# Optimization experiments

Measured on AMD Instinct MI355X. Metric: run time of the kernel, lower is better.

The kernel has to match this reference:

```python
import jax, jax.numpy as jnp
import numpy as np

D_EMB = 1024
N_H = 16
D_H = D_EMB // N_H

def setup_inputs() -> dict:
    key = jax.random.key(0)
    ks = jax.random.split(key, 9)
    s = 1.0 / np.sqrt(D_EMB)
    inp = {"x": jax.random.normal(ks[0], (2, 2048, D_EMB), dtype=jnp.float32)}
    for i, name in enumerate(["q", "k", "v", "o"]):
        inp[f"W{name}"] = jax.random.uniform(ks[1 + 2 * i], (D_EMB, D_EMB), minval=-s, maxval=s, dtype=jnp.float32)
        inp[f"b{name}"] = jax.random.uniform(ks[2 + 2 * i], (D_EMB,), minval=-s, maxval=s, dtype=jnp.float32)
    return inp

def reference(x, Wq, bq, Wk, bk, Wv, bv, Wo, bo):
    B, S, D = x.shape
    # torch Linear: y = x @ W.T + b
    Q = x @ Wq.T + bq
    K = x @ Wk.T + bk
    V = x @ Wv.T + bv
    # [B, H, S, d_h]
    Qh = Q.reshape(B, S, N_H, D_H).transpose(0, 2, 1, 3)
    Kh = K.reshape(B, S, N_H, D_H).transpose(0, 2, 1, 3)
    Vh = V.reshape(B, S, N_H, D_H).transpose(0, 2, 1, 3)
    scores = jnp.einsum("bhsd,bhtd->bhst", Qh, Kh) / jnp.sqrt(jnp.float32(D_H))
    causal = jnp.tril(jnp.ones((S, S), dtype=bool))
    scores = jnp.where(causal, scores, -jnp.inf)
    attn = jax.nn.softmax(scores, axis=-1)
    out = jnp.einsum("bhst,bhtd->bhsd", attn, Vh)
    out = out.transpose(0, 2, 1, 3).reshape(B, S, D)
    return out @ Wo.T + bo
```

## Files before the change

kernel.cpp:

```cpp
#include <hip/hip_runtime.h>
#include <stdint.h>

#define B_  2
#define S_  2048
#define D_  1024
#define H_  16
#define DH_ 64
#define M_  (B_ * S_)

#define NEG_BIG   (-1.0e30f)
#define EXP_FLOOR (-60.0f)
#define FIXED_M   16.0f

typedef uint16_t u16;
typedef uint32_t u32;
typedef u16   u16x4  __attribute__((ext_vector_type(4)));
typedef u16   u16x8  __attribute__((ext_vector_type(8)));
typedef u32   u32x4  __attribute__((ext_vector_type(4)));
typedef __bf16 bf16_t;
typedef bf16_t bf16x8 __attribute__((ext_vector_type(8)));
typedef float floatx4 __attribute__((ext_vector_type(4)));

__device__ __forceinline__ u16 f2b(float f) {
  u32 u = __float_as_uint(f);
  return (u16)((u + 0x7FFFu + ((u >> 16) & 1u)) >> 16);
}
__device__ __forceinline__ bf16x8 bc8(u16x8 v) { return __builtin_bit_cast(bf16x8, v); }

__device__ __forceinline__ void async16(u16* lds, const u16* g) {
  __builtin_amdgcn_global_load_lds(
      (const __attribute__((address_space(1))) u32*)g,
      (__attribute__((address_space(3))) u32*)lds, 16, 0, 0);
}

__global__ __launch_bounds__(256) void cvt_kernel(
    const float* __restrict__ X,
    const float* __restrict__ Wq, const float* __restrict__ Wk,
    const float* __restrict__ Wv, const float* __restrict__ Wo,
    u16* __restrict__ Xb, u16* __restrict__ Wqb, u16* __restrict__ Wkb,
    u16* __restrict__ Wvb, u16* __restrict__ Wob)
{
  const int XC = (M_ * D_) / 8;
  const int WC = (D_ * D_) / 8;
  const int total = XC + 4 * WC;
  for (int cid = blockIdx.x * 256 + threadIdx.x; cid < total; cid += gridDim.x * 256) {
    const float* src; u16* dst; int off;
    if (cid < XC)               { src = X;  dst = Xb;  off = cid; }
    else if (cid < XC + WC)     { src = Wq; dst = Wqb; off = cid - XC; }
    else if (cid < XC + 2 * WC) { src = Wk; dst = Wkb; off = cid - XC - WC; }
    else if (cid < XC + 3 * WC) { src = Wv; dst = Wvb; off = cid - XC - 2 * WC; }
    else                        { src = Wo; dst = Wob; off = cid - XC - 3 * WC; }
    const float4* p = (const float4*)(src + (size_t)off * 8);
    float4 lo = p[0], hi = p[1];
    u16x8 o;
    o[0] = f2b(lo.x); o[1] = f2b(lo.y); o[2] = f2b(lo.z); o[3] = f2b(lo.w);
    o[4] = f2b(hi.x); o[5] = f2b(hi.y); o[6] = f2b(hi.z); o[7] = f2b(hi.w);
    *(u16x8*)(dst + (size_t)off * 8) = o;
  }
}

__global__ __launch_bounds__(256) void qkv_kernel(
    const u16* __restrict__ Xb,
    const u16* __restrict__ Wqb, const u16* __restrict__ Wkb, const u16* __restrict__ Wvb,
    const float* __restrict__ bq, const float* __restrict__ bk, const float* __restrict__ bv,
    u16* __restrict__ Qb, u16* __restrict__ Kb, u16* __restrict__ Vb)
{
  const int which = blockIdx.y >> 3;
  const u16* W      = (which == 0) ? Wqb : (which == 1) ? Wkb : Wvb;
  const float* bias = (which == 0) ? bq : (which == 1) ? bk : bv;
  u16* Y            = (which == 0) ? Qb : (which == 1) ? Kb : Vb;
  const int gm = blockIdx.x * 128;
  const int gn = (blockIdx.y & 7) * 128;

  __shared__ u16 Al[2][128][32];
  __shared__ u16 Bl[2][128][32];

  const int t  = threadIdx.x;
  const int wv = t >> 6, ln = t & 63;
  const int c  = ln & 15, g = ln >> 4;
  const int wm = (wv >> 1) * 64, wn = (wv & 1) * 64;

  const int srow   = ln >> 2;
  const int schunk = (ln & 3) ^ ((ln >> 3) & 3);
  const u16* a0 = Xb + (size_t)(gm + wv * 16 + srow) * D_ + schunk * 8;
  const u16* a1 = a0 + (size_t)64 * D_;
  const u16* b0 = W  + (size_t)(gn + wv * 16 + srow) * D_ + schunk * 8;
  const u16* b1 = b0 + (size_t)64 * D_;

  floatx4 acc[4][4] = {};
  const int rsw = (c >> 1) & 3;

  async16(&Al[0][wv * 16][0],      a0);
  async16(&Al[0][64 + wv * 16][0], a1);
  async16(&Bl[0][wv * 16][0],      b0);
  async16(&Bl[0][64 + wv * 16][0], b1);

  for (int kt = 0; kt < D_ / 32; ++kt) {
    __syncthreads();
    if (kt + 1 < D_ / 32) {
      const int nb = (kt + 1) & 1;
      const int ko = (kt + 1) * 32;
      async16(&Al[nb][wv * 16][0],      a0 + ko);
      async16(&Al[nb][64 + wv * 16][0], a1 + ko);
      async16(&Bl[nb][wv * 16][0],      b0 + ko);
      async16(&Bl[nb][64 + wv * 16][0], b1 + ko);
    }
    const int bf = kt & 1;
    bf16x8 am[4], bn[4];
#pragma unroll
    for (int i = 0; i < 4; ++i) {
      am[i] = bc8(*(const u16x8*)&Al[bf][wm + 16 * i + c][(g ^ rsw) * 8]);
      bn[i] = bc8(*(const u16x8*)&Bl[bf][wn + 16 * i + c][(g ^ rsw) * 8]);
    }
#pragma unroll
    for (int mi = 0; mi < 4; ++mi)
#pragma unroll
      for (int ni = 0; ni < 4; ++ni)
        acc[mi][ni] = __builtin_amdgcn_mfma_f32_16x16x32_bf16(am[mi], bn[ni], acc[mi][ni], 0, 0, 0);
  }

#pragma unroll
  for (int ni = 0; ni < 4; ++ni) {
    const int col = gn + wn + 16 * ni + c;
    const float bv_ = bias[col];
#pragma unroll
    for (int mi = 0; mi < 4; ++mi)
#pragma unroll
      for (int r = 0; r < 4; ++r)
        Y[(size_t)(gm + wm + 16 * mi + 4 * g + r) * D_ + col] = f2b(acc[mi][ni][r] + bv_);
  }
}

__global__ __launch_bounds__(256) void proj_kernel(
    const u16* __restrict__ A, const u16* __restrict__ Wb,
    const float* __restrict__ bias, float* __restrict__ Y)
{
  const int gm = blockIdx.x * 64;
  const int gn = blockIdx.y * 128;

  __shared__ u16 Al[2][64][32];
  __shared__ u16 Bl[2][128][32];

  const int t  = threadIdx.x;
  const int wv = t >> 6, ln = t & 63;
  const int c  = ln & 15, g = ln >> 4;
  const int wm = (wv >> 1) * 32, wn = (wv & 1) * 64;

  const int srow   = ln >> 2;
  const int schunk = (ln & 3) ^ ((ln >> 3) & 3);
  const u16* a0 = A  + (size_t)(gm + wv * 16 + srow) * D_ + schunk * 8;
  const u16* b0 = Wb + (size_t)(gn + wv * 16 + srow) * D_ + schunk * 8;
  const u16* b1 = b0 + (size_t)64 * D_;

  floatx4 acc[2][4] = {};
  const int rsw = (c >> 1) & 3;

  async16(&Al[0][wv * 16][0],      a0);
  async16(&Bl[0][wv * 16][0],      b0);
  async16(&Bl[0][64 + wv * 16][0], b1);

  for (int kt = 0; kt < D_ / 32; ++kt) {
    __syncthreads();
    if (kt + 1 < D_ / 32) {
      const int nb = (kt + 1) & 1;
      const int ko = (kt + 1) * 32;
      async16(&Al[nb][wv * 16][0],      a0 + ko);
      async16(&Bl[nb][wv * 16][0],      b0 + ko);
      async16(&Bl[nb][64 + wv * 16][0], b1 + ko);
    }
    const int bf = kt & 1;
    bf16x8 am[2], bn[4];
#pragma unroll
    for (int i = 0; i < 2; ++i)
      am[i] = bc8(*(const u16x8*)&Al[bf][wm + 16 * i + c][(g ^ rsw) * 8]);
#pragma unroll
    for (int i = 0; i < 4; ++i)
      bn[i] = bc8(*(const u16x8*)&Bl[bf][wn + 16 * i + c][(g ^ rsw) * 8]);
#pragma unroll
    for (int mi = 0; mi < 2; ++mi)
#pragma unroll
      for (int ni = 0; ni < 4; ++ni)
        acc[mi][ni] = __builtin_amdgcn_mfma_f32_16x16x32_bf16(am[mi], bn[ni], acc[mi][ni], 0, 0, 0);
  }

#pragma unroll
  for (int ni = 0; ni < 4; ++ni) {
    const int col = gn + wn + 16 * ni + c;
    const float bv_ = bias[col];
#pragma unroll
    for (int mi = 0; mi < 2; ++mi)
#pragma unroll
      for (int r = 0; r < 4; ++r)
        Y[(size_t)(gm + wm + 16 * mi + 4 * g + r) * D_ + col] = acc[mi][ni][r] + bv_;
  }
}

__global__ __launch_bounds__(256) void attn_kernel(
    const u16* __restrict__ Qg, const u16* __restrict__ Kg,
    const u16* __restrict__ Vg, u16* __restrict__ Og)
{
  const int bh = blockIdx.x;
  const int b = bh >> 4, h = bh & 15;
  const int qb = 31 - blockIdx.y;
  const int q0 = qb * 64;

  __shared__ u16 Kl[64][72];
  __shared__ u16 Vt[64][72];

  const int t = threadIdx.x;
  const int wave = t >> 6, lane = t & 63;
  const int c = lane & 15, g = lane >> 4;
  const int qrow = q0 + wave * 16 + c;

  bf16x8 qf[2];
  {
    const u16* qsrc = Qg + (size_t)(b * S_ + qrow) * D_ + h * DH_ + 8 * g;
    qf[0] = bc8(*(const u16x8*)qsrc);
    qf[1] = bc8(*(const u16x8*)(qsrc + 32));
  }

  float l_run = 0.f;
  floatx4 o[4] = {};

  const int kr = t >> 2, kc = (t & 3) * 16;
  const int vkp = t & 31, vdg = t >> 5;

  u16x8 kreg0, kreg1;
  u32 vpack[8];
  {
    const u16* ksrc = Kg + (size_t)(b * S_ + kr) * D_ + h * DH_ + kc;
    kreg0 = *(const u16x8*)ksrc;
    kreg1 = *(const u16x8*)(ksrc + 8);
    const u16* vsrc = Vg + (size_t)(b * S_ + 2 * vkp) * D_ + h * DH_ + 8 * vdg;
    u16x8 va = *(const u16x8*)vsrc;
    u16x8 vb2 = *(const u16x8*)(vsrc + D_);
#pragma unroll
    for (int i = 0; i < 8; ++i) vpack[i] = (u32)va[i] | ((u32)vb2[i] << 16);
  }

  for (int kt = 0; kt <= qb; ++kt) {
    const int k0 = kt * 64;
    __syncthreads();
    *(u16x8*)&Kl[kr][kc]     = kreg0;
    *(u16x8*)&Kl[kr][kc + 8] = kreg1;
#pragma unroll
    for (int i = 0; i < 8; ++i) *(u32*)&Vt[8 * vdg + i][2 * vkp] = vpack[i];
    __syncthreads();

    if (kt < qb) {
      const u16* ksrc = Kg + (size_t)(b * S_ + k0 + 64 + kr) * D_ + h * DH_ + kc;
      kreg0 = *(const u16x8*)ksrc;
      kreg1 = *(const u16x8*)(ksrc + 8);
      const u16* vsrc = Vg + (size_t)(b * S_ + k0 + 64 + 2 * vkp) * D_ + h * DH_ + 8 * vdg;
      u16x8 va = *(const u16x8*)vsrc;
      u16x8 vb2 = *(const u16x8*)(vsrc + D_);
#pragma unroll
      for (int i = 0; i < 8; ++i) vpack[i] = (u32)va[i] | ((u32)vb2[i] << 16);
    }

    floatx4 st[4] = {};
#pragma unroll
    for (int mb = 0; mb < 4; ++mb) {
      bf16x8 a0 = bc8(*(const u16x8*)&Kl[16 * mb + c][8 * g]);
      bf16x8 a1 = bc8(*(const u16x8*)&Kl[16 * mb + c][32 + 8 * g]);
      st[mb] = __builtin_amdgcn_mfma_f32_16x16x32_bf16(a0, qf[0], st[mb], 0, 0, 0);
      st[mb] = __builtin_amdgcn_mfma_f32_16x16x32_bf16(a1, qf[1], st[mb], 0, 0, 0);
    }

    u32 plo[4], phi[4];
    float psum = 0.f;
    const bool diag = (kt == qb);
#pragma unroll
    for (int mb = 0; mb < 4; ++mb) {
      u32 pb[4];
#pragma unroll
      for (int r = 0; r < 4; ++r) {
        float arg = fmaf(st[mb][r], 0.125f, -FIXED_M);
        if (diag && (k0 + 16 * mb + 4 * g + r > qrow)) arg = NEG_BIG;
        arg = fmaxf(arg, EXP_FLOOR);
        float p = __expf(arg);
        pb[r] = __float_as_uint(p) & 0xFFFF0000u;
        psum += __uint_as_float(pb[r]);
      }
      plo[mb] = (pb[0] >> 16) | pb[1];
      phi[mb] = (pb[2] >> 16) | pb[3];
    }
    l_run += psum;

    const int s1 = c + 32 * (g & 1);
    const int s2 = s1 + 16;
    const bool hi = (g >= 2);
#pragma unroll
    for (int ks = 0; ks < 2; ++ks) {
      u32 q0a = (u32)__shfl((int)plo[2 * ks],     s1);
      u32 q1a = (u32)__shfl((int)phi[2 * ks],     s1);
      u32 q2a = (u32)__shfl((int)plo[2 * ks],     s2);
      u32 q3a = (u32)__shfl((int)phi[2 * ks],     s2);
      u32 q0b = (u32)__shfl((int)plo[2 * ks + 1], s1);
      u32 q1b = (u32)__shfl((int)phi[2 * ks + 1], s1);
      u32 q2b = (u32)__shfl((int)plo[2 * ks + 1], s2);
      u32 q3b = (u32)__shfl((int)phi[2 * ks + 1], s2);
      u32x4 pa = { hi ? q0b : q0a, hi ? q1b : q1a, hi ? q2b : q2a, hi ? q3b : q3a };
      bf16x8 pfrag = __builtin_bit_cast(bf16x8, pa);
#pragma unroll
      for (int nb = 0; nb < 4; ++nb) {
        bf16x8 vf = bc8(*(const u16x8*)&Vt[16 * nb + c][32 * ks + 8 * g]);
        o[nb] = __builtin_amdgcn_mfma_f32_16x16x32_bf16(vf, pfrag, o[nb], 0, 0, 0);
      }
    }
  }

  l_run += __shfl_xor(l_run, 16);
  l_run += __shfl_xor(l_run, 32);
  const float inv = 1.0f / l_run;
#pragma unroll
  for (int nb = 0; nb < 4; ++nb) {
    u16x4 ov;
#pragma unroll
    for (int r = 0; r < 4; ++r) ov[r] = f2b(o[nb][r] * inv);
    *(u16x4*)(Og + (size_t)(b * S_ + qrow) * D_ + h * DH_ + 16 * nb + 4 * g) = ov;
  }
}

extern "C" void kernel_launch(void* const* d_in, const int* in_sizes, int n_in,
                              void* d_out, int out_size, void* d_ws, size_t ws_size,
                              hipStream_t stream) {
  const float* x  = (const float*)d_in[0];
  const float* Wq = (const float*)d_in[1];
  const float* bq = (const float*)d_in[2];
  const float* Wk = (const float*)d_in[3];
  const float* bk = (const float*)d_in[4];
  const float* Wv = (const float*)d_in[5];
  const float* bv = (const float*)d_in[6];
  const float* Wo = (const float*)d_in[7];
  const float* bo = (const float*)d_in[8];

  u16* Xb  = (u16*)d_ws;
  u16* Wqb = Xb  + (size_t)M_ * D_;
  u16* Wkb = Wqb + (size_t)D_ * D_;
  u16* Wvb = Wkb + (size_t)D_ * D_;
  u16* Wob = Wvb + (size_t)D_ * D_;
  u16* Qb  = Wob + (size_t)D_ * D_;
  u16* Vb  = (u16*)d_out;
  u16* Kb  = Vb + (size_t)M_ * D_;

  cvt_kernel<<<dim3(2048), 256, 0, stream>>>(x, Wq, Wk, Wv, Wo, Xb, Wqb, Wkb, Wvb, Wob);
  qkv_kernel<<<dim3(32, 24), 256, 0, stream>>>(Xb, Wqb, Wkb, Wvb, bq, bk, bv, Qb, Kb, Vb);
  attn_kernel<<<dim3(B_ * H_, 32), 256, 0, stream>>>(Qb, Kb, Vb, Qb);
  proj_kernel<<<dim3(64, 8), 256, 0, stream>>>(Qb, Wob, bo, (float*)d_out);
}
```

Before: 194.0 us.

## Process two query sub-tiles per wave in attention with fewer threads

The attention kernel now runs 2 waves per block instead of 4, and each wave handles 32 query rows (two 16-row subtiles). K and V fragments loaded from LDS are reused across both subtiles, and each thread stages twice as much K/V data. The softmax uses exp2 with a pre-scaled constant, drops the exponent floor clamp, converts to bf16 with a packed hardware convert, and is specialised for diagonal versus off-diagonal tiles. The permutation shuffle is reworked to need 4 shuffles per subtile instead of 8. Register pressure rises and there are fewer waves per block to hide latency.

```diff
diff --git a/kernel.cpp b/kernel.cpp
--- a/kernel.cpp
+++ b/kernel.cpp
@@ -9,7 +9,6 @@
 #define M_  (B_ * S_)
 
 #define NEG_BIG   (-1.0e30f)
-#define EXP_FLOOR (-60.0f)
 #define FIXED_M   16.0f
 
 typedef uint16_t u16;
@@ -195,7 +194,7 @@
   }
 }
 
-__global__ __launch_bounds__(256) void attn_kernel(
+__global__ __launch_bounds__(128) void attn_kernel(
     const u16* __restrict__ Qg, const u16* __restrict__ Kg,
     const u16* __restrict__ Vg, u16* __restrict__ Og)
 {
@@ -208,117 +207,149 @@
   __shared__ u16 Vt[64][72];
 
   const int t = threadIdx.x;
-  const int wave = t >> 6, lane = t & 63;
+  const int w = t >> 6, lane = t & 63;
   const int c = lane & 15, g = lane >> 4;
-  const int qrow = q0 + wave * 16 + c;
-
-  bf16x8 qf[2];
-  {
-    const u16* qsrc = Qg + (size_t)(b * S_ + qrow) * D_ + h * DH_ + 8 * g;
-    qf[0] = bc8(*(const u16x8*)qsrc);
-    qf[1] = bc8(*(const u16x8*)(qsrc + 32));
-  }
-
-  float l_run = 0.f;
-  floatx4 o[4] = {};
-
-  const int kr = t >> 2, kc = (t & 3) * 16;
+  const int qbase = q0 + 32 * w;
+
+  const float C1 = 0.125f * 1.44269504f;
+  const float C2 = -FIXED_M * 1.44269504f;
+
+  bf16x8 qf[2][2];
+#pragma unroll
+  for (int qs = 0; qs < 2; ++qs) {
+    const u16* qsrc = Qg + (size_t)(b * S_ + qbase + 16 * qs + c) * D_ + h * DH_ + 8 * g;
+    qf[qs][0] = bc8(*(const u16x8*)qsrc);
+    qf[qs][1] = bc8(*(const u16x8*)(qsrc + 32));
+  }
+
+  float l_run[2] = {0.f, 0.f};
+  floatx4 o[2][4] = {};
+
+  const int kr = t >> 1, kc = (t & 1) * 32;
   const int vkp = t & 31, vdg = t >> 5;
 
-  u16x8 kreg0, kreg1;
-  u32 vpack[8];
+  u16x8 kreg[4];
+  u32 vpack[16];
   {
     const u16* ksrc = Kg + (size_t)(b * S_ + kr) * D_ + h * DH_ + kc;
-    kreg0 = *(const u16x8*)ksrc;
-    kreg1 = *(const u16x8*)(ksrc + 8);
-    const u16* vsrc = Vg + (size_t)(b * S_ + 2 * vkp) * D_ + h * DH_ + 8 * vdg;
-    u16x8 va = *(const u16x8*)vsrc;
-    u16x8 vb2 = *(const u16x8*)(vsrc + D_);
-#pragma unroll
-    for (int i = 0; i < 8; ++i) vpack[i] = (u32)va[i] | ((u32)vb2[i] << 16);
-  }
+#pragma unroll
+    for (int i = 0; i < 4; ++i) kreg[i] = *(const u16x8*)(ksrc + 8 * i);
+    const u16* vsrc = Vg + (size_t)(b * S_ + 2 * vkp) * D_ + h * DH_ + 16 * vdg;
+    u16x8 va0 = *(const u16x8*)vsrc;
+    u16x8 va1 = *(const u16x8*)(vsrc + 8);
+    u16x8 vb0 = *(const u16x8*)(vsrc + D_);
+    u16x8 vb1 = *(const u16x8*)(vsrc + D_ + 8);
+#pragma unroll
+    for (int i = 0; i < 8; ++i) {
+      vpack[i]     = (u32)va0[i] | ((u32)vb0[i] << 16);
+      vpack[8 + i] = (u32)va1[i] | ((u32)vb1[i] << 16);
+    }
+  }
+
+  u32 plo[2][4], phi[2][4];
 
   for (int kt = 0; kt <= qb; ++kt) {
     const int k0 = kt * 64;
     __syncthreads();
-    *(u16x8*)&Kl[kr][kc]     = kreg0;
-    *(u16x8*)&Kl[kr][kc + 8] = kreg1;
-#pragma unroll
-    for (int i = 0; i < 8; ++i) *(u32*)&Vt[8 * vdg + i][2 * vkp] = vpack[i];
+#pragma unroll
+    for (int i = 0; i < 4; ++i) *(u16x8*)&Kl[kr][kc + 8 * i] = kreg[i];
+#pragma unroll
+    for (int i = 0; i < 16; ++i) *(u32*)&Vt[16 * vdg + i][2 * vkp] = vpack[i];
     __syncthreads();
 
     if (kt < qb) {
       const u16* ksrc = Kg + (size_t)(b * S_ + k0 + 64 + kr) * D_ + h * DH_ + kc;
-      kreg0 = *(const u16x8*)ksrc;
-      kreg1 = *(const u16x8*)(ksrc + 8);
-      const u16* vsrc = Vg + (size_t)(b * S_ + k0 + 64 + 2 * vkp) * D_ + h * DH_ + 8 * vdg;
-      u16x8 va = *(const u16x8*)vsrc;
-      u16x8 vb2 = *(const u16x8*)(vsrc + D_);
-#pragma unroll
-      for (int i = 0; i < 8; ++i) vpack[i] = (u32)va[i] | ((u32)vb2[i] << 16);
-    }
-
-    floatx4 st[4] = {};
+#pragma unroll
+      for (int i = 0; i < 4; ++i) kreg[i] = *(const u16x8*)(ksrc + 8 * i);
+      const u16* vsrc = Vg + (size_t)(b * S_ + k0 + 64 + 2 * vkp) * D_ + h * DH_ + 16 * vdg;
+      u16x8 va0 = *(const u16x8*)vsrc;
+      u16x8 va1 = *(const u16x8*)(vsrc + 8);
+      u16x8 vb0 = *(const u16x8*)(vsrc + D_);
+      u16x8 vb1 = *(const u16x8*)(vsrc + D_ + 8);
+#pragma unroll
+      for (int i = 0; i < 8; ++i) {
+        vpack[i]     = (u32)va0[i] | ((u32)vb0[i] << 16);
+        vpack[8 + i] = (u32)va1[i] | ((u32)vb1[i] << 16);
+      }
+    }
+
+    floatx4 st[2][4] = {};
 #pragma unroll
     for (int mb = 0; mb < 4; ++mb) {
       bf16x8 a0 = bc8(*(const u16x8*)&Kl[16 * mb + c][8 * g]);
       bf16x8 a1 = bc8(*(const u16x8*)&Kl[16 * mb + c][32 + 8 * g]);
-      st[mb] = __builtin_amdgcn_mfma_f32_16x16x32_bf16(a0, qf[0], st[mb], 0, 0, 0);
-      st[mb] = __builtin_amdgcn_mfma_f32_16x16x32_bf16(a1, qf[1], st[mb], 0, 0, 0);
-    }
-
-    u32 plo[4], phi[4];
-    float psum = 0.f;
-    const bool diag = (kt == qb);
-#pragma unroll
-    for (int mb = 0; mb < 4; ++mb) {
-      u32 pb[4];
-#pragma unroll
-      for (int r = 0; r < 4; ++r) {
-        float arg = fmaf(st[mb][r], 0.125f, -FIXED_M);
-        if (diag && (k0 + 16 * mb + 4 * g + r > qrow)) arg = NEG_BIG;
-        arg = fmaxf(arg, EXP_FLOOR);
-        float p = __expf(arg);
-        pb[r] = __float_as_uint(p) & 0xFFFF0000u;
-        psum += __uint_as_float(pb[r]);
+      st[0][mb] = __builtin_amdgcn_mfma_f32_16x16x32_bf16(a0, qf[0][0], st[0][mb], 0, 0, 0);
+      st[0][mb] = __builtin_amdgcn_mfma_f32_16x16x32_bf16(a1, qf[0][1], st[0][mb], 0, 0, 0);
+      st[1][mb] = __builtin_amdgcn_mfma_f32_16x16x32_bf16(a0, qf[1][0], st[1][mb], 0, 0, 0);
+      st[1][mb] = __builtin_amdgcn_mfma_f32_16x16x32_bf16(a1, qf[1][1], st[1][mb], 0, 0, 0);
+    }
+
+    auto softmax = [&](bool DIAG) {
+#pragma unroll
+      for (int qs = 0; qs < 2; ++qs) {
+        const int qrow_ = qbase + 16 * qs + c;
+        float psum = 0.f;
+#pragma unroll
+        for (int mb = 0; mb < 4; ++mb) {
+          float p[4];
+#pragma unroll
+          for (int r = 0; r < 4; ++r) {
+            float arg = fmaf(st[qs][mb][r], C1, C2);
+            if (DIAG && (k0 + 16 * mb + 4 * g + r > qrow_)) arg = NEG_BIG;
+            p[r] = __builtin_exp2f(arg);
+            psum += p[r];
+          }
+          asm("v_cvt_pk_bf16_f32 %0, %1, %2" : "=v"(plo[qs][mb]) : "v"(p[0]), "v"(p[1]));
+          asm("v_cvt_pk_bf16_f32 %0, %1, %2" : "=v"(phi[qs][mb]) : "v"(p[2]), "v"(p[3]));
+        }
+        l_run[qs] += psum;
       }
-      plo[mb] = (pb[0] >> 16) | pb[1];
-      phi[mb] = (pb[2] >> 16) | pb[3];
-    }
-    l_run += psum;
-
-    const int s1 = c + 32 * (g & 1);
-    const int s2 = s1 + 16;
-    const bool hi = (g >= 2);
+    };
+    if (kt == qb) softmax(true); else softmax(false);
+
+    const int gb = g & 1, gh = g >> 1;
+    const int aA = c + 32 * gb + 16 * gh;
+    const int aB = c + 32 * gb + 16 * (1 - gh);
 #pragma unroll
     for (int ks = 0; ks < 2; ++ks) {
-      u32 q0a = (u32)__shfl((int)plo[2 * ks],     s1);
-      u32 q1a = (u32)__shfl((int)phi[2 * ks],     s1);
-      u32 q2a = (u32)__shfl((int)plo[2 * ks],     s2);
-      u32 q3a = (u32)__shfl((int)phi[2 * ks],     s2);
-      u32 q0b = (u32)__shfl((int)plo[2 * ks + 1], s1);
-      u32 q1b = (u32)__shfl((int)phi[2 * ks + 1], s1);
-      u32 q2b = (u32)__shfl((int)plo[2 * ks + 1], s2);
-      u32 q3b = (u32)__shfl((int)phi[2 * ks + 1], s2);
-      u32x4 pa = { hi ? q0b : q0a, hi ? q1b : q1a, hi ? q2b : q2a, hi ? q3b : q3a };
-      bf16x8 pfrag = __builtin_bit_cast(bf16x8, pa);
+      bf16x8 pfrag[2];
+#pragma unroll
+      for (int qs = 0; qs < 2; ++qs) {
+        u32 x0 = gb ? plo[qs][2 * ks + 1] : plo[qs][2 * ks];
+        u32 x1 = gb ? phi[qs][2 * ks + 1] : phi[qs][2 * ks];
+        u32 x2 = gb ? plo[qs][2 * ks]     : plo[qs][2 * ks + 1];
+        u32 x3 = gb ? phi[qs][2 * ks]     : phi[qs][2 * ks + 1];
+        u32 i0 = (u32)__shfl((int)x0, aA);
+        u32 i1 = (u32)__shfl((int)x1, aA);
+        u32 i2 = (u32)__shfl((int)x2, aB);
+        u32 i3 = (u32)__shfl((int)x3, aB);
+        const bool sw = (gh != 0);
+        u32x4 pa = { sw ? i2 : i0, sw ? i3 : i1, sw ? i0 : i2, sw ? i1 : i3 };
+        pfrag[qs] = __builtin_bit_cast(bf16x8, pa);
+      }
 #pragma unroll
       for (int nb = 0; nb < 4; ++nb) {
         bf16x8 vf = bc8(*(const u16x8*)&Vt[16 * nb + c][32 * ks + 8 * g]);
-        o[nb] = __builtin_amdgcn_mfma_f32_16x16x32_bf16(vf, pfrag, o[nb], 0, 0, 0);
+        o[0][nb] = __builtin_amdgcn_mfma_f32_16x16x32_bf16(vf, pfrag[0], o[0][nb], 0, 0, 0);
+        o[1][nb] = __builtin_amdgcn_mfma_f32_16x16x32_bf16(vf, pfrag[1], o[1][nb], 0, 0, 0);
       }
     }
   }
 
-  l_run += __shfl_xor(l_run, 16);
-  l_run += __shfl_xor(l_run, 32);
-  const float inv = 1.0f / l_run;
-#pragma unroll
-  for (int nb = 0; nb < 4; ++nb) {
-    u16x4 ov;
-#pragma unroll
-    for (int r = 0; r < 4; ++r) ov[r] = f2b(o[nb][r] * inv);
-    *(u16x4*)(Og + (size_t)(b * S_ + qrow) * D_ + h * DH_ + 16 * nb + 4 * g) = ov;
+#pragma unroll
+  for (int qs = 0; qs < 2; ++qs) {
+    float l = l_run[qs];
+    l += __shfl_xor(l, 16);
+    l += __shfl_xor(l, 32);
+    const float inv = 1.0f / l;
+    const int qrow_ = qbase + 16 * qs + c;
+#pragma unroll
+    for (int nb = 0; nb < 4; ++nb) {
+      u16x4 ov;
+#pragma unroll
+      for (int r = 0; r < 4; ++r) ov[r] = f2b(o[qs][nb][r] * inv);
+      *(u16x4*)(Og + (size_t)(b * S_ + qrow_) * D_ + h * DH_ + 16 * nb + 4 * g) = ov;
+    }
   }
 }
 
@@ -346,6 +377,6 @@
 
   cvt_kernel<<<dim3(2048), 256, 0, stream>>>(x, Wq, Wk, Wv, Wo, Xb, Wqb, Wkb, Wvb, Wob);
   qkv_kernel<<<dim3(32, 24), 256, 0, stream>>>(Xb, Wqb, Wkb, Wvb, bq, bk, bv, Qb, Kb, Vb);
-  attn_kernel<<<dim3(B_ * H_, 32), 256, 0, stream>>>(Qb, Kb, Vb, Qb);
+  attn_kernel<<<dim3(B_ * H_, 32), 128, 0, stream>>>(Qb, Kb, Vb, Qb);
   proj_kernel<<<dim3(64, 8), 256, 0, stream>>>(Qb, Wob, bo, (float*)d_out);
 }
```

Measured after the change: 207.2 us. 6.8% more time.

## Double-buffer K/V LDS tiles and streamline softmax exp and P shuffles

Applied to the files above, without the earlier changes.

Double-buffers the K and V LDS tiles so each iteration needs one barrier instead of two, letting stores for the next tile proceed without waiting on readers of the previous one. The softmax is rewritten to use exp2 with pre-folded log2e constants, drops the exp floor clamp, and converts pairs with the hardware packed bf16 conversion instead of truncation masks. A mask-free softmax variant is used for non-diagonal tiles. The P redistribution halves the number of cross-lane shuffles by pre-selecting sources. Rounding now differs slightly from truncation, and removing the clamp relies on exp2 underflowing cleanly to zero.

```diff
diff --git a/kernel.cpp b/kernel.cpp
--- a/kernel.cpp
+++ b/kernel.cpp
@@ -9,7 +9,6 @@
 #define M_  (B_ * S_)
 
 #define NEG_BIG   (-1.0e30f)
-#define EXP_FLOOR (-60.0f)
 #define FIXED_M   16.0f
 
 typedef uint16_t u16;
@@ -204,13 +203,16 @@
   const int qb = 31 - blockIdx.y;
   const int q0 = qb * 64;
 
-  __shared__ u16 Kl[64][72];
-  __shared__ u16 Vt[64][72];
+  __shared__ u16 Kl[2][64][72];
+  __shared__ u16 Vt[2][64][72];
 
   const int t = threadIdx.x;
   const int wave = t >> 6, lane = t & 63;
   const int c = lane & 15, g = lane >> 4;
   const int qrow = q0 + wave * 16 + c;
+
+  const float C1 = 0.125f * 1.44269504f;
+  const float C2 = -FIXED_M * 1.44269504f;
 
   bf16x8 qf[2];
   {
@@ -225,86 +227,85 @@
   const int kr = t >> 2, kc = (t & 3) * 16;
   const int vkp = t & 31, vdg = t >> 5;
 
-  u16x8 kreg0, kreg1;
-  u32 vpack[8];
+  u16x8 kreg0, kreg1, va, vb2;
   {
     const u16* ksrc = Kg + (size_t)(b * S_ + kr) * D_ + h * DH_ + kc;
     kreg0 = *(const u16x8*)ksrc;
     kreg1 = *(const u16x8*)(ksrc + 8);
     const u16* vsrc = Vg + (size_t)(b * S_ + 2 * vkp) * D_ + h * DH_ + 8 * vdg;
-    u16x8 va = *(const u16x8*)vsrc;
-    u16x8 vb2 = *(const u16x8*)(vsrc + D_);
-#pragma unroll
-    for (int i = 0; i < 8; ++i) vpack[i] = (u32)va[i] | ((u32)vb2[i] << 16);
+    va  = *(const u16x8*)vsrc;
+    vb2 = *(const u16x8*)(vsrc + D_);
   }
 
   for (int kt = 0; kt <= qb; ++kt) {
     const int k0 = kt * 64;
-    __syncthreads();
-    *(u16x8*)&Kl[kr][kc]     = kreg0;
-    *(u16x8*)&Kl[kr][kc + 8] = kreg1;
-#pragma unroll
-    for (int i = 0; i < 8; ++i) *(u32*)&Vt[8 * vdg + i][2 * vkp] = vpack[i];
-    __syncthreads();
+    const int bf = kt & 1;
+
+    *(u16x8*)&Kl[bf][kr][kc]     = kreg0;
+    *(u16x8*)&Kl[bf][kr][kc + 8] = kreg1;
+#pragma unroll
+    for (int i = 0; i < 8; ++i)
+      *(u32*)&Vt[bf][8 * vdg + i][2 * vkp] = (u32)va[i] | ((u32)vb2[i] << 16);
 
     if (kt < qb) {
       const u16* ksrc = Kg + (size_t)(b * S_ + k0 + 64 + kr) * D_ + h * DH_ + kc;
       kreg0 = *(const u16x8*)ksrc;
       kreg1 = *(const u16x8*)(ksrc + 8);
       const u16* vsrc = Vg + (size_t)(b * S_ + k0 + 64 + 2 * vkp) * D_ + h * DH_ + 8 * vdg;
-      u16x8 va = *(const u16x8*)vsrc;
-      u16x8 vb2 = *(const u16x8*)(vsrc + D_);
-#pragma unroll
-      for (int i = 0; i < 8; ++i) vpack[i] = (u32)va[i] | ((u32)vb2[i] << 16);
-    }
+      va  = *(const u16x8*)vsrc;
+      vb2 = *(const u16x8*)(vsrc + D_);
+    }
+
+    __syncthreads();
 
     floatx4 st[4] = {};
 #pragma unroll
     for (int mb = 0; mb < 4; ++mb) {
-      bf16x8 a0 = bc8(*(const u16x8*)&Kl[16 * mb + c][8 * g]);
-      bf16x8 a1 = bc8(*(const u16x8*)&Kl[16 * mb + c][32 + 8 * g]);
+      bf16x8 a0 = bc8(*(const u16x8*)&Kl[bf][16 * mb + c][8 * g]);
+      bf16x8 a1 = bc8(*(const u16x8*)&Kl[bf][16 * mb + c][32 + 8 * g]);
       st[mb] = __builtin_amdgcn_mfma_f32_16x16x32_bf16(a0, qf[0], st[mb], 0, 0, 0);
       st[mb] = __builtin_amdgcn_mfma_f32_16x16x32_bf16(a1, qf[1], st[mb], 0, 0, 0);
     }
 
     u32 plo[4], phi[4];
-    float psum = 0.f;
-    const bool diag = (kt == qb);
-#pragma unroll
-    for (int mb = 0; mb < 4; ++mb) {
-      u32 pb[4];
-#pragma unroll
-      for (int r = 0; r < 4; ++r) {
-        float arg = fmaf(st[mb][r], 0.125f, -FIXED_M);
-        if (diag && (k0 + 16 * mb + 4 * g + r > qrow)) arg = NEG_BIG;
-        arg = fmaxf(arg, EXP_FLOOR);
-        float p = __expf(arg);
-        pb[r] = __float_as_uint(p) & 0xFFFF0000u;
-        psum += __uint_as_float(pb[r]);
+    auto softmax = [&](bool DIAG) {
+      float psum = 0.f;
+#pragma unroll
+      for (int mb = 0; mb < 4; ++mb) {
+        float p[4];
+#pragma unroll
+        for (int r = 0; r < 4; ++r) {
+          float arg = fmaf(st[mb][r], C1, C2);
+          if (DIAG && (k0 + 16 * mb + 4 * g + r > qrow)) arg = NEG_BIG;
+          p[r] = __builtin_exp2f(arg);
+          psum += p[r];
+        }
+        asm("v_cvt_pk_bf16_f32 %0, %1, %2" : "=v"(plo[mb]) : "v"(p[0]), "v"(p[1]));
+        asm("v_cvt_pk_bf16_f32 %0, %1, %2" : "=v"(phi[mb]) : "v"(p[2]), "v"(p[3]));
       }
-      plo[mb] = (pb[0] >> 16) | pb[1];
-      phi[mb] = (pb[2] >> 16) | pb[3];
-    }
-    l_run += psum;
-
-    const int s1 = c + 32 * (g & 1);
-    const int s2 = s1 + 16;
-    const bool hi = (g >= 2);
+      l_run += psum;
+    };
+    if (kt == qb) softmax(true); else softmax(false);
+
+    const int gb = g & 1, gh = g >> 1;
+    const int aA = c + 32 * gb + 16 * gh;
+    const int aB = c + 32 * gb + 16 * (1 - gh);
 #pragma unroll
     for (int ks = 0; ks < 2; ++ks) {
-      u32 q0a = (u32)__shfl((int)plo[2 * ks],     s1);
-      u32 q1a = (u32)__shfl((int)phi[2 * ks],     s1);
-      u32 q2a = (u32)__shfl((int)plo[2 * ks],     s2);
-      u32 q3a = (u32)__shfl((int)phi[2 * ks],     s2);
-      u32 q0b = (u32)__shfl((int)plo[2 * ks + 1], s1);
-      u32 q1b = (u32)__shfl((int)phi[2 * ks + 1], s1);
-      u32 q2b = (u32)__shfl((int)plo[2 * ks + 1], s2);
-      u32 q3b = (u32)__shfl((int)phi[2 * ks + 1], s2);
-      u32x4 pa = { hi ? q0b : q0a, hi ? q1b : q1a, hi ? q2b : q2a, hi ? q3b : q3a };
+      u32 x0 = gb ? plo[2 * ks + 1] : plo[2 * ks];
+      u32 x1 = gb ? phi[2 * ks + 1] : phi[2 * ks];
+      u32 x2 = gb ? plo[2 * ks]     : plo[2 * ks + 1];
+      u32 x3 = gb ? phi[2 * ks]     : phi[2 * ks + 1];
+      u32 i0 = (u32)__shfl((int)x0, aA);
+      u32 i1 = (u32)__shfl((int)x1, aA);
+      u32 i2 = (u32)__shfl((int)x2, aB);
+      u32 i3 = (u32)__shfl((int)x3, aB);
+      const bool sw = (gh != 0);
+      u32x4 pa = { sw ? i2 : i0, sw ? i3 : i1, sw ? i0 : i2, sw ? i1 : i3 };
       bf16x8 pfrag = __builtin_bit_cast(bf16x8, pa);
 #pragma unroll
       for (int nb = 0; nb < 4; ++nb) {
-        bf16x8 vf = bc8(*(const u16x8*)&Vt[16 * nb + c][32 * ks + 8 * g]);
+        bf16x8 vf = bc8(*(const u16x8*)&Vt[bf][16 * nb + c][32 * ks + 8 * g]);
         o[nb] = __builtin_amdgcn_mfma_f32_16x16x32_bf16(vf, pfrag, o[nb], 0, 0, 0);
       }
     }
```

After: 187.7 us. 3.3% less time.
